# Kernel tuning notes

Measured on AMD Instinct MI355X. Metric: run time of the kernel, lower is better.

## Reference

```python
import jax, jax.numpy as jnp
import numpy as np

NEG_SLOPE = 0.2


def gat_layer(x, src, dst, W, a_src, a_dst, bias, heads, ch, n):
    # x: [N, F_in]; W: [F_in, heads*ch]; a_src/a_dst: [heads, ch]; bias: [heads*ch]
    h = (x @ W).reshape(n, heads, ch)                      # [N, H, C]
    e_src = (h * a_src[None]).sum(-1)                      # [N, H]
    e_dst = (h * a_dst[None]).sum(-1)                      # [N, H]
    e = jax.nn.leaky_relu(e_src[src] + e_dst[dst], NEG_SLOPE)  # [E, H]
    # segment softmax over incoming edges of each dst node
    m = jax.ops.segment_max(e, dst, num_segments=n)        # [N, H]
    e = jnp.exp(e - m[dst])
    denom = jax.ops.segment_sum(e, dst, num_segments=n)    # [N, H]
    alpha = e / (denom[dst] + 1e-16)                       # [E, H]
    msg = h[src] * alpha[:, :, None]                       # [E, H, C]
    out = jax.ops.segment_sum(msg, dst, num_segments=n)    # [N, H, C]
    return out.reshape(n, heads * ch) + bias


def setup_inputs() -> dict:
    key = jax.random.key(0)
    ks = jax.random.split(key, 12)
    N, E, F_IN, C, H = 50000, 1600000, 128, 64, 4
    x = jax.random.normal(ks[0], (N, F_IN), dtype=jnp.float32)
    edge_index = jax.random.randint(ks[1], (2, E), 0, N, dtype=jnp.int32)
    s = 0.1
    return {
        "x": x,
        "edge_index": edge_index,
        "W1": jax.random.normal(ks[2], (F_IN, H * C), dtype=jnp.float32) * s,
        "a_src1": jax.random.normal(ks[3], (H, C), dtype=jnp.float32) * s,
        "a_dst1": jax.random.normal(ks[4], (H, C), dtype=jnp.float32) * s,
        "b1": jnp.zeros((H * C,), dtype=jnp.float32),
        "W2": jax.random.normal(ks[5], (H * C, C), dtype=jnp.float32) * s,
        "a_src2": jax.random.normal(ks[6], (1, C), dtype=jnp.float32) * s,
        "a_dst2": jax.random.normal(ks[7], (1, C), dtype=jnp.float32) * s,
        "b2": jnp.zeros((C,), dtype=jnp.float32),
        "Wout": jax.random.normal(ks[8], (C, 1), dtype=jnp.float32) * s,
        "bout": jnp.zeros((1,), dtype=jnp.float32),
    }


def reference(x, edge_index, W1, a_src1, a_dst1, b1, W2, a_src2, a_dst2, b2, Wout, bout):
    n = x.shape[0]
    # PyG GATConv default add_self_loops=True
    loop = jnp.arange(n, dtype=edge_index.dtype)
    src = jnp.concatenate([edge_index[0], loop])
    dst = jnp.concatenate([edge_index[1], loop])
    h = gat_layer(x, src, dst, W1, a_src1, a_dst1, b1, heads=4, ch=64, n=n)
    h = jax.nn.relu(h)
    h = gat_layer(h, src, dst, W2, a_src2, a_dst2, b2, heads=1, ch=64, n=n)
    h = jax.nn.relu(h)
    logits = (h @ Wout + bout).squeeze(-1)  # [N]
    return logits
```

## Files before the change

### kernel.cpp

```cpp
#include <hip/hip_runtime.h>
#include <hip/hip_bf16.h>

#define NEG_SLOPE 0.2f

using bf16x8 = __attribute__((ext_vector_type(8))) short;
using f32x4  = __attribute__((ext_vector_type(4))) float;

__device__ __forceinline__ unsigned short f2b(float f) {
  unsigned int u = __float_as_uint(f);
  unsigned int r = (u + 0x7FFFu + ((u >> 16) & 1u)) >> 16;
  return (unsigned short)r;
}
__device__ __forceinline__ float b2f(unsigned short v) {
  return __uint_as_float(((unsigned int)v) << 16);
}
__device__ __forceinline__ float leaky_exp(float e) {
  e = e > 0.f ? e : NEG_SLOPE * e;
  return __expf(e);
}

__global__ void k_prep(const float* __restrict__ W1,
                       const float* __restrict__ W2,
                       const float* __restrict__ a_src1,
                       const float* __restrict__ a_dst1,
                       unsigned short* __restrict__ W1h,
                       unsigned short* __restrict__ W1l,
                       unsigned short* __restrict__ W2h,
                       unsigned short* __restrict__ W2l,
                       float* __restrict__ va) {
  int b = blockIdx.x;
  int t = threadIdx.x;
  if (b < 16) {
    int g = b * 256 + t;
    int l = g & 63, tt = (g >> 6) & 3, kc = (g >> 8) & 3, h = (g >> 10) & 3;
    int n = h * 64 + tt * 16 + (l & 15);
    int kbase = kc * 32 + (l >> 4) * 8;
    size_t base = ((((size_t)h * 4 + kc) * 4 + tt) * 64 + l) * 8;
#pragma unroll
    for (int j = 0; j < 8; j++) {
      float v = W1[(size_t)(kbase + j) * 256 + n];
      unsigned short hi = f2b(v);
      W1h[base + j] = hi;
      W1l[base + j] = f2b(v - b2f(hi));
    }
  } else if (b < 24) {
    int g = (b - 16) * 256 + t;
    int l = g & 63, tt = (g >> 6) & 3, kc = (g >> 8) & 7;
    int n = tt * 16 + (l & 15);
    int kbase = kc * 32 + (l >> 4) * 8;
    size_t base = (((size_t)kc * 4 + tt) * 64 + l) * 8;
#pragma unroll
    for (int j = 0; j < 8; j++) {
      float v = W2[(size_t)(kbase + j) * 64 + n];
      unsigned short hi = f2b(v);
      W2h[base + j] = hi;
      W2l[base + j] = f2b(v - b2f(hi));
    }
  } else {
    int g = (b - 24) * 256 + t;
    int k = g >> 3, j = g & 7;
    int h = j & 3;
    const float* a = (j < 4) ? a_src1 : a_dst1;
    float s = 0.f;
    for (int c = 0; c < 64; c++) s += W1[(size_t)k * 256 + h * 64 + c] * a[h * 64 + c];
    va[k * 8 + j] = s;
  }
}

__global__ __launch_bounds__(256) void k_gh_mfma(const unsigned short* __restrict__ Ab,
                                                 const unsigned short* __restrict__ W1h,
                                                 const unsigned short* __restrict__ W1l,
                                                 const float* __restrict__ b1,
                                                 unsigned short* __restrict__ hact_hi,
                                                 unsigned short* __restrict__ hact_lo,
                                                 int M) {
  const int w = threadIdx.x >> 6, l = threadIdx.x & 63;
  const int h = blockIdx.z;
  const int rowA = blockIdx.x * 64 + w * 16 + (l & 15);
  const int rA = rowA < M ? rowA : M - 1;
  const int kg = l >> 4;
  const unsigned short* Aptr = Ab + (size_t)rA * 512 + h * 128 + kg * 8;
  f32x4 acc[4] = {{0.f, 0.f, 0.f, 0.f}, {0.f, 0.f, 0.f, 0.f},
                  {0.f, 0.f, 0.f, 0.f}, {0.f, 0.f, 0.f, 0.f}};
#pragma unroll
  for (int kc = 0; kc < 4; kc++) {
    bf16x8 a = *reinterpret_cast<const bf16x8*>(Aptr + kc * 32);
#pragma unroll
    for (int t = 0; t < 4; t++) {
      size_t base = ((((size_t)h * 4 + kc) * 4 + t) * 64 + l) * 8;
      bf16x8 bh = *reinterpret_cast<const bf16x8*>(W1h + base);
      bf16x8 bl = *reinterpret_cast<const bf16x8*>(W1l + base);
      acc[t] = __builtin_amdgcn_mfma_f32_16x16x32_bf16(a, bh, acc[t], 0, 0, 0);
      acc[t] = __builtin_amdgcn_mfma_f32_16x16x32_bf16(a, bl, acc[t], 0, 0, 0);
    }
  }
  const int orow0 = blockIdx.x * 64 + w * 16 + (l >> 4) * 4;
  const int col16 = l & 15;
#pragma unroll
  for (int t = 0; t < 4; t++) {
    int col = h * 64 + t * 16 + col16;
    float bb = b1[col];
#pragma unroll
    for (int r = 0; r < 4; r++) {
      int row = orow0 + r;
      if (row < M) {
        float v = fmaxf(acc[t][r] + bb, 0.f);
        unsigned short hi = f2b(v);
        hact_hi[(size_t)row * 256 + col] = hi;
        hact_lo[(size_t)row * 256 + col] = f2b(v - b2f(hi));
      }
    }
  }
}

__global__ __launch_bounds__(256) void k_g2_mfma(const unsigned short* __restrict__ Ahi,
                                                 const unsigned short* __restrict__ Alo,
                                                 const unsigned short* __restrict__ W2h,
                                                 const unsigned short* __restrict__ W2l,
                                                 unsigned short* __restrict__ h2b,
                                                 int M) {
  const int w = threadIdx.x >> 6, l = threadIdx.x & 63;
  const int rowA = blockIdx.x * 64 + w * 16 + (l & 15);
  const int rA = rowA < M ? rowA : M - 1;
  const int kg = l >> 4;
  const unsigned short* Ah = Ahi + (size_t)rA * 256 + kg * 8;
  const unsigned short* Al = Alo + (size_t)rA * 256 + kg * 8;
  f32x4 acc[4] = {{0.f, 0.f, 0.f, 0.f}, {0.f, 0.f, 0.f, 0.f},
                  {0.f, 0.f, 0.f, 0.f}, {0.f, 0.f, 0.f, 0.f}};
#pragma unroll
  for (int kc = 0; kc < 8; kc++) {
    bf16x8 ah = *reinterpret_cast<const bf16x8*>(Ah + kc * 32);
    bf16x8 al = *reinterpret_cast<const bf16x8*>(Al + kc * 32);
#pragma unroll
    for (int t = 0; t < 4; t++) {
      size_t base = (((size_t)kc * 4 + t) * 64 + l) * 8;
      bf16x8 bh = *reinterpret_cast<const bf16x8*>(W2h + base);
      bf16x8 bl = *reinterpret_cast<const bf16x8*>(W2l + base);
      acc[t] = __builtin_amdgcn_mfma_f32_16x16x32_bf16(ah, bh, acc[t], 0, 0, 0);
      acc[t] = __builtin_amdgcn_mfma_f32_16x16x32_bf16(ah, bl, acc[t], 0, 0, 0);
      acc[t] = __builtin_amdgcn_mfma_f32_16x16x32_bf16(al, bh, acc[t], 0, 0, 0);
    }
  }
  const int orow0 = blockIdx.x * 64 + w * 16 + (l >> 4) * 4;
  const int col16 = l & 15;
#pragma unroll
  for (int t = 0; t < 4; t++) {
    int col = t * 16 + col16;
#pragma unroll
    for (int r = 0; r < 4; r++) {
      int row = orow0 + r;
      if (row < M) h2b[(size_t)row * 64 + col] = f2b(acc[t][r]);
    }
  }
}

__global__ __launch_bounds__(256) void k_scores_x(const float* __restrict__ x,
                                                  const float* __restrict__ va,
                                                  float* __restrict__ s_src,
                                                  float* __restrict__ s_dst,
                                                  unsigned short* __restrict__ xb,
                                                  int N) {
  int n = blockIdx.x * 4 + (threadIdx.x >> 6);
  if (n >= N) return;
  int lane = threadIdx.x & 63;
  float x0 = x[(size_t)n * 128 + lane];
  float x1 = x[(size_t)n * 128 + 64 + lane];
  xb[(size_t)n * 128 + lane] = f2b(x0);
  xb[(size_t)n * 128 + 64 + lane] = f2b(x1);
  float4 vs0 = *reinterpret_cast<const float4*>(va + lane * 8);
  float4 vd0 = *reinterpret_cast<const float4*>(va + lane * 8 + 4);
  float4 vs1 = *reinterpret_cast<const float4*>(va + (lane + 64) * 8);
  float4 vd1 = *reinterpret_cast<const float4*>(va + (lane + 64) * 8 + 4);
  float rs0 = x0 * vs0.x + x1 * vs1.x, rs1 = x0 * vs0.y + x1 * vs1.y;
  float rs2 = x0 * vs0.z + x1 * vs1.z, rs3 = x0 * vs0.w + x1 * vs1.w;
  float rd0 = x0 * vd0.x + x1 * vd1.x, rd1 = x0 * vd0.y + x1 * vd1.y;
  float rd2 = x0 * vd0.z + x1 * vd1.z, rd3 = x0 * vd0.w + x1 * vd1.w;
#pragma unroll
  for (int off = 32; off; off >>= 1) {
    rs0 += __shfl_xor(rs0, off, 64); rs1 += __shfl_xor(rs1, off, 64);
    rs2 += __shfl_xor(rs2, off, 64); rs3 += __shfl_xor(rs3, off, 64);
    rd0 += __shfl_xor(rd0, off, 64); rd1 += __shfl_xor(rd1, off, 64);
    rd2 += __shfl_xor(rd2, off, 64); rd3 += __shfl_xor(rd3, off, 64);
  }
  if (lane == 0) {
    float4 ss = {rs0, rs1, rs2, rs3};
    float4 dd = {rd0, rd1, rd2, rd3};
    *reinterpret_cast<float4*>(s_src + (size_t)n * 4) = ss;
    *reinterpret_cast<float4*>(s_dst + (size_t)n * 4) = dd;
  }
}

__global__ __launch_bounds__(256) void k_scores2(const unsigned short* __restrict__ h2b,
                                                 const float* __restrict__ a_src,
                                                 const float* __restrict__ a_dst,
                                                 float* __restrict__ s_src,
                                                 float* __restrict__ s_dst,
                                                 int N) {
  int n = blockIdx.x * 4 + (threadIdx.x >> 6);
  if (n >= N) return;
  int lane = threadIdx.x & 63;
  float hv = b2f(h2b[(size_t)n * 64 + lane]);
  float sv = hv * a_src[lane];
  float dv = hv * a_dst[lane];
#pragma unroll
  for (int off = 32; off; off >>= 1) {
    sv += __shfl_xor(sv, off, 64);
    dv += __shfl_xor(dv, off, 64);
  }
  if (lane == 0) {
    s_src[n] = sv;
    s_dst[n] = dv;
  }
}

__global__ void k_histA(const int* __restrict__ ei, int E, int Etot,
                        int* __restrict__ ghist) {
  __shared__ int lh[256];
  int t = threadIdx.x;
  lh[t] = 0;
  __syncthreads();
  int base = (blockIdx.x * 256 + t) * 8;
#pragma unroll
  for (int j = 0; j < 8; j++) {
    int e = base + j;
    if (e < Etot) {
      int dst = (e < E) ? ei[E + e] : (e - E);
      atomicAdd(&lh[dst >> 8], 1);
    }
  }
  __syncthreads();
  if (lh[t]) atomicAdd(&ghist[t], lh[t]);
}

__global__ __launch_bounds__(256) void k_scan196(const int* __restrict__ ghist,
                                                 int* __restrict__ bstart,
                                                 int* __restrict__ gcur,
                                                 int nbuck, int Etot) {
  __shared__ int ws[4];
  int t = threadIdx.x;
  int lane = t & 63, wid = t >> 6;
  int v = (t < nbuck) ? ghist[t] : 0;
  int x = v;
#pragma unroll
  for (int off = 1; off < 64; off <<= 1) {
    int y = __shfl_up(x, off, 64);
    if (lane >= off) x += y;
  }
  if (lane == 63) ws[wid] = x;
  __syncthreads();
  if (t == 0) {
    int a0 = ws[0], a1 = ws[1], a2 = ws[2];
    ws[0] = 0; ws[1] = a0; ws[2] = a0 + a1; ws[3] = a0 + a1 + a2;
  }
  __syncthreads();
  int excl = x - v + ws[wid];
  if (t < nbuck) {
    bstart[t] = excl;
    gcur[t] = excl;
  }
  if (t == 0) bstart[nbuck] = Etot;
}

__global__ void k_scatterA(const int* __restrict__ ei, int E, int Etot,
                           int* __restrict__ gcur,
                           int* __restrict__ keys1,
                           int* __restrict__ vals1) {
  __shared__ int lh[256];
  int t = threadIdx.x;
  lh[t] = 0;
  __syncthreads();
  int base = (blockIdx.x * 256 + t) * 8;
  int dsts[8], srcs[8];
#pragma unroll
  for (int j = 0; j < 8; j++) {
    int e = base + j;
    if (e < Etot) {
      int d, s;
      if (e < E) { d = ei[E + e]; s = ei[e]; }
      else       { d = s = e - E; }
      dsts[j] = d; srcs[j] = s;
      atomicAdd(&lh[d >> 8], 1);
    } else dsts[j] = -1;
  }
  __syncthreads();
  {
    int c = lh[t];
    lh[t] = c ? atomicAdd(&gcur[t], c) : 0;
  }
  __syncthreads();
#pragma unroll
  for (int j = 0; j < 8; j++) {
    if (dsts[j] >= 0) {
      int pos = atomicAdd(&lh[dsts[j] >> 8], 1);
      keys1[pos] = dsts[j];
      vals1[pos] = srcs[j];
    }
  }
}

__global__ __launch_bounds__(256) void k_sortB(const int* __restrict__ keys1,
                                               const int* __restrict__ vals1,
                                               const int* __restrict__ bstart,
                                               int* __restrict__ src_sorted,
                                               int* __restrict__ row_ptr,
                                               int N, int Etot) {
  __shared__ int lh[256];
  __shared__ int ws[4];
  int b = blockIdx.x;
  int t = threadIdx.x;
  int lane = t & 63, wid = t >> 6;
  int s = bstart[b], e2 = bstart[b + 1];
  lh[t] = 0;
  __syncthreads();
  for (int p = s + t; p < e2; p += 256)
    atomicAdd(&lh[keys1[p] & 255], 1);
  __syncthreads();
  int v = lh[t];
  int x = v;
#pragma unroll
  for (int off = 1; off < 64; off <<= 1) {
    int y = __shfl_up(x, off, 64);
    if (lane >= off) x += y;
  }
  if (lane == 63) ws[wid] = x;
  __syncthreads();
  if (t == 0) {
    int a0 = ws[0], a1 = ws[1], a2 = ws[2];
    ws[0] = 0; ws[1] = a0; ws[2] = a0 + a1; ws[3] = a0 + a1 + a2;
  }
  __syncthreads();
  int excl = x - v + ws[wid];
  int dst = (b << 8) + t;
  if (dst < N) row_ptr[dst] = s + excl;
  __syncthreads();
  lh[t] = s + excl;
  __syncthreads();
  for (int p = s + t; p < e2; p += 256) {
    int k = keys1[p] & 255;
    int pos = atomicAdd(&lh[k], 1);
    src_sorted[pos] = vals1[p];
  }
  if (b == 0 && t == 0) row_ptr[N] = Etot;
}

__global__ __launch_bounds__(256) void k_w1csr(const int* __restrict__ row_ptr,
                                               const int* __restrict__ src_sorted,
                                               const float* __restrict__ s_src,
                                               const float* __restrict__ s_dst,
                                               float4* __restrict__ w1s, int N) {
  int n = blockIdx.x * 4 + (threadIdx.x >> 6);
  if (n >= N) return;
  int lane = threadIdx.x & 63;
  float4 sd = *reinterpret_cast<const float4*>(s_dst + (size_t)n * 4);
  int beg = row_ptr[n], end = row_ptr[n + 1];
  for (int p = beg + lane; p < end; p += 64) {
    int s = src_sorted[p];
    float4 ss = *reinterpret_cast<const float4*>(s_src + (size_t)s * 4);
    float4 w;
    w.x = leaky_exp(ss.x + sd.x);
    w.y = leaky_exp(ss.y + sd.y);
    w.z = leaky_exp(ss.z + sd.z);
    w.w = leaky_exp(ss.w + sd.w);
    w1s[p] = w;
  }
}

__global__ __launch_bounds__(256) void k_w2csr(const int* __restrict__ row_ptr,
                                               const int* __restrict__ src_sorted,
                                               const float* __restrict__ s2s,
                                               const float* __restrict__ s2d,
                                               float* __restrict__ w2s, int N) {
  int n = blockIdx.x * 4 + (threadIdx.x >> 6);
  if (n >= N) return;
  int lane = threadIdx.x & 63;
  float sdn = s2d[n];
  int beg = row_ptr[n], end = row_ptr[n + 1];
  for (int p = beg + lane; p < end; p += 64) {
    w2s[p] = leaky_exp(s2s[src_sorted[p]] + sdn);
  }
}

__global__ __launch_bounds__(256) void k_aggx(const unsigned short* __restrict__ xb,
                                              const int* __restrict__ row_ptr,
                                              const int* __restrict__ src_sorted,
                                              const float4* __restrict__ w1s,
                                              unsigned short* __restrict__ avgxb,
                                              int N) {
  int n = blockIdx.x * 4 + (threadIdx.x >> 6);
  if (n >= N) return;
  int lane = threadIdx.x & 63;
  int beg = row_ptr[n], end = row_ptr[n + 1];
  float acc[4][2] = {};
  float wsum[4] = {};
  int p = beg;
  for (; p + 4 <= end; p += 4) {
    int s[4];
    float4 w[4];
    unsigned int pk[4];
#pragma unroll
    for (int j = 0; j < 4; j++) s[j] = src_sorted[p + j];
#pragma unroll
    for (int j = 0; j < 4; j++) w[j] = w1s[p + j];
#pragma unroll
    for (int j = 0; j < 4; j++)
      pk[j] = *reinterpret_cast<const unsigned int*>(xb + (size_t)s[j] * 128 + lane * 2);
#pragma unroll
    for (int j = 0; j < 4; j++) {
      float x0 = __uint_as_float(pk[j] << 16);
      float x1 = __uint_as_float(pk[j] & 0xFFFF0000u);
      acc[0][0] = fmaf(w[j].x, x0, acc[0][0]); acc[0][1] = fmaf(w[j].x, x1, acc[0][1]);
      acc[1][0] = fmaf(w[j].y, x0, acc[1][0]); acc[1][1] = fmaf(w[j].y, x1, acc[1][1]);
      acc[2][0] = fmaf(w[j].z, x0, acc[2][0]); acc[2][1] = fmaf(w[j].z, x1, acc[2][1]);
      acc[3][0] = fmaf(w[j].w, x0, acc[3][0]); acc[3][1] = fmaf(w[j].w, x1, acc[3][1]);
      wsum[0] += w[j].x; wsum[1] += w[j].y; wsum[2] += w[j].z; wsum[3] += w[j].w;
    }
  }
  for (; p < end; p++) {
    int s = src_sorted[p];
    float4 w = w1s[p];
    unsigned int pk = *reinterpret_cast<const unsigned int*>(xb + (size_t)s * 128 + lane * 2);
    float x0 = __uint_as_float(pk << 16);
    float x1 = __uint_as_float(pk & 0xFFFF0000u);
    acc[0][0] = fmaf(w.x, x0, acc[0][0]); acc[0][1] = fmaf(w.x, x1, acc[0][1]);
    acc[1][0] = fmaf(w.y, x0, acc[1][0]); acc[1][1] = fmaf(w.y, x1, acc[1][1]);
    acc[2][0] = fmaf(w.z, x0, acc[2][0]); acc[2][1] = fmaf(w.z, x1, acc[2][1]);
    acc[3][0] = fmaf(w.w, x0, acc[3][0]); acc[3][1] = fmaf(w.w, x1, acc[3][1]);
    wsum[0] += w.x; wsum[1] += w.y; wsum[2] += w.z; wsum[3] += w.w;
  }
#pragma unroll
  for (int h = 0; h < 4; h++) {
    float inv = 1.f / (wsum[h] + 1e-16f);
    unsigned int pk = ((unsigned int)f2b(acc[h][1] * inv) << 16) | f2b(acc[h][0] * inv);
    *reinterpret_cast<unsigned int*>(avgxb + (size_t)n * 512 + h * 128 + lane * 2) = pk;
  }
}

__global__ __launch_bounds__(256) void k_agg2(const unsigned short* __restrict__ h2b,
                                              const int* __restrict__ row_ptr,
                                              const int* __restrict__ src_sorted,
                                              const float* __restrict__ w2s,
                                              const float* __restrict__ bias,
                                              const float* __restrict__ Wout,
                                              const float* __restrict__ bout,
                                              float* __restrict__ logits, int N) {
  int n = blockIdx.x * 4 + (threadIdx.x >> 6);
  if (n >= N) return;
  int lane = threadIdx.x & 63;
  int beg = row_ptr[n], end = row_ptr[n + 1];
  float acc = 0.f, wsum = 0.f;
  int p = beg;
  for (; p + 8 <= end; p += 8) {
    int s[8];
    float w[8];
    unsigned short hv[8];
#pragma unroll
    for (int j = 0; j < 8; j++) s[j] = src_sorted[p + j];
#pragma unroll
    for (int j = 0; j < 8; j++) w[j] = w2s[p + j];
#pragma unroll
    for (int j = 0; j < 8; j++) hv[j] = h2b[(size_t)s[j] * 64 + lane];
#pragma unroll
    for (int j = 0; j < 8; j++) {
      acc = fmaf(w[j], b2f(hv[j]), acc);
      wsum += w[j];
    }
  }
  for (; p < end; p++) {
    float w = w2s[p];
    acc = fmaf(w, b2f(h2b[(size_t)src_sorted[p] * 64 + lane]), acc);
    wsum += w;
  }
  float o = fmaxf(acc / (wsum + 1e-16f) + bias[lane], 0.f);
  float v = o * Wout[lane];
#pragma unroll
  for (int off = 32; off; off >>= 1) v += __shfl_xor(v, off, 64);
  if (lane == 0) logits[n] = v + bout[0];
}

extern "C" void kernel_launch(void* const* d_in, const int* in_sizes, int n_in,
                              void* d_out, int out_size, void* d_ws, size_t ws_size,
                              hipStream_t stream) {
  const float* x      = (const float*)d_in[0];
  const int*   ei     = (const int*)d_in[1];
  const float* W1     = (const float*)d_in[2];
  const float* a_src1 = (const float*)d_in[3];
  const float* a_dst1 = (const float*)d_in[4];
  const float* b1     = (const float*)d_in[5];
  const float* W2     = (const float*)d_in[6];
  const float* a_src2 = (const float*)d_in[7];
  const float* a_dst2 = (const float*)d_in[8];
  const float* b2     = (const float*)d_in[9];
  const float* Wout   = (const float*)d_in[10];
  const float* bout   = (const float*)d_in[11];
  float* logits = (float*)d_out;

  const int HC1  = in_sizes[5];
  const int F_IN = in_sizes[2] / HC1;
  const int N    = in_sizes[0] / F_IN;
  const int E    = in_sizes[1] / 2;
  const int Etot = E + N;
  const int NBUCK = (N + 255) >> 8;

  char* w = (char*)d_ws;
  auto alloc = [&](size_t bytes) {
    char* p = w;
    w += (bytes + 255) & ~(size_t)255;
    return p;
  };
  char* regA = alloc((size_t)N * 128 * sizeof(unsigned short));
  unsigned short* xb = (unsigned short*)regA;
  char* regB = alloc((size_t)N * 512 * sizeof(unsigned short));
  unsigned short* avgxb = (unsigned short*)regB;
  unsigned short* h2b = (unsigned short*)regB;
  float* w2s = (float*)(regB + (size_t)N * 256 * sizeof(unsigned short));
  char* regC = alloc((size_t)N * 256 * 4);
  int* keys1 = (int*)regC;
  int* vals1 = (int*)(regC + (size_t)Etot * 4 + 256);
  float4* w1s = (float4*)regC;
  unsigned short* hact_hi = (unsigned short*)regC;
  unsigned short* hact_lo = (unsigned short*)(regC + (size_t)N * 256 * sizeof(unsigned short));
  float* s_src1  = (float*)alloc((size_t)N * 4 * 4);
  float* s_dst1  = (float*)alloc((size_t)N * 4 * 4);
  float* s2_src  = (float*)alloc((size_t)N * 4);
  float* s2_dst  = (float*)alloc((size_t)N * 4);
  float* va      = (float*)alloc(128 * 8 * 4);
  unsigned short* W1h = (unsigned short*)alloc(4096 * 8 * 2);
  unsigned short* W1l = (unsigned short*)alloc(4096 * 8 * 2);
  unsigned short* W2h = (unsigned short*)alloc(2048 * 8 * 2);
  unsigned short* W2l = (unsigned short*)alloc(2048 * 8 * 2);
  int* row_ptr   = (int*)alloc((size_t)(N + 1) * 4);
  int* src_sorted= (int*)alloc((size_t)Etot * 4);
  int* ghist     = (int*)alloc(256 * 4);
  int* bstart    = (int*)alloc(260 * 4);
  int* gcur      = (int*)alloc(256 * 4);

  hipMemsetAsync(ghist, 0, 256 * 4, stream);

  k_prep<<<28, 256, 0, stream>>>(W1, W2, a_src1, a_dst1, W1h, W1l, W2h, W2l, va);
  k_scores_x<<<(N + 3) / 4, 256, 0, stream>>>(x, va, s_src1, s_dst1, xb, N);

  const int gsort = (Etot + 2047) / 2048;
  k_histA<<<gsort, 256, 0, stream>>>(ei, E, Etot, ghist);
  k_scan196<<<1, 256, 0, stream>>>(ghist, bstart, gcur, NBUCK, Etot);
  k_scatterA<<<gsort, 256, 0, stream>>>(ei, E, Etot, gcur, keys1, vals1);
  k_sortB<<<NBUCK, 256, 0, stream>>>(keys1, vals1, bstart, src_sorted, row_ptr, N, Etot);

  k_w1csr<<<(N + 3) / 4, 256, 0, stream>>>(row_ptr, src_sorted, s_src1, s_dst1, w1s, N);
  k_aggx<<<(N + 3) / 4, 256, 0, stream>>>(xb, row_ptr, src_sorted, w1s, avgxb, N);
  dim3 gh((N + 63) / 64, 1, 4);
  k_gh_mfma<<<gh, 256, 0, stream>>>(avgxb, W1h, W1l, b1, hact_hi, hact_lo, N);

  k_g2_mfma<<<(N + 63) / 64, 256, 0, stream>>>(hact_hi, hact_lo, W2h, W2l, h2b, N);
  k_scores2<<<(N + 3) / 4, 256, 0, stream>>>(h2b, a_src2, a_dst2, s2_src, s2_dst, N);
  k_w2csr<<<(N + 3) / 4, 256, 0, stream>>>(row_ptr, src_sorted, s2_src, s2_dst, w2s, N);
  k_agg2<<<(N + 3) / 4, 256, 0, stream>>>(h2b, row_ptr, src_sorted, w2s,
                                          b2, Wout, bout, logits, N);
}
```

Before: 425.3 us.

## Fuse histogram into scores kernel, pre-normalize attention weights, widen aggx unroll

Drops the memset by zeroing the histogram inside k_prep, and merges the destination histogram into the x-scores kernel as extra blocks, removing two launches. The edge-weight kernels now compute the per-node softmax denominator with a wave reduction and write normalized weights. This takes the weight sums and divides out of both aggregation loops, at the cost of a second pass over the weights (cached in registers for up to 256 edges). The layer-1 aggregation unroll goes from 4 to 8 edges to expose more memory-level parallelism.

```diff
diff --git a/kernel.cpp b/kernel.cpp
--- a/kernel.cpp
+++ b/kernel.cpp
@@ -27,7 +27,8 @@
                        unsigned short* __restrict__ W1l,
                        unsigned short* __restrict__ W2h,
                        unsigned short* __restrict__ W2l,
-                       float* __restrict__ va) {
+                       float* __restrict__ va,
+                       int* __restrict__ ghist) {
   int b = blockIdx.x;
   int t = threadIdx.x;
   if (b < 16) {
@@ -56,7 +57,7 @@
       W2h[base + j] = hi;
       W2l[base + j] = f2b(v - b2f(hi));
     }
-  } else {
+  } else if (b < 28) {
     int g = (b - 24) * 256 + t;
     int k = g >> 3, j = g & 7;
     int h = j & 3;
@@ -64,6 +65,8 @@
     float s = 0.f;
     for (int c = 0; c < 64; c++) s += W1[(size_t)k * 256 + h * 64 + c] * a[h * 64 + c];
     va[k * 8 + j] = s;
+  } else {
+    ghist[t] = 0;
   }
 }
 
@@ -154,12 +157,33 @@
   }
 }
 
-__global__ __launch_bounds__(256) void k_scores_x(const float* __restrict__ x,
-                                                  const float* __restrict__ va,
-                                                  float* __restrict__ s_src,
-                                                  float* __restrict__ s_dst,
-                                                  unsigned short* __restrict__ xb,
-                                                  int N) {
+__global__ __launch_bounds__(256) void k_sxh(const float* __restrict__ x,
+                                             const float* __restrict__ va,
+                                             float* __restrict__ s_src,
+                                             float* __restrict__ s_dst,
+                                             unsigned short* __restrict__ xb,
+                                             int N, int nsx,
+                                             const int* __restrict__ ei,
+                                             int E, int Etot,
+                                             int* __restrict__ ghist) {
+  __shared__ int lh[256];
+  if (blockIdx.x >= nsx) {
+    int t = threadIdx.x;
+    lh[t] = 0;
+    __syncthreads();
+    int base = ((blockIdx.x - nsx) * 256 + t) * 8;
+#pragma unroll
+    for (int j = 0; j < 8; j++) {
+      int e = base + j;
+      if (e < Etot) {
+        int dst = (e < E) ? ei[E + e] : (e - E);
+        atomicAdd(&lh[dst >> 8], 1);
+      }
+    }
+    __syncthreads();
+    if (lh[t]) atomicAdd(&ghist[t], lh[t]);
+    return;
+  }
   int n = blockIdx.x * 4 + (threadIdx.x >> 6);
   if (n >= N) return;
   int lane = threadIdx.x & 63;
@@ -213,25 +237,6 @@
   }
 }
 
-__global__ void k_histA(const int* __restrict__ ei, int E, int Etot,
-                        int* __restrict__ ghist) {
-  __shared__ int lh[256];
-  int t = threadIdx.x;
-  lh[t] = 0;
-  __syncthreads();
-  int base = (blockIdx.x * 256 + t) * 8;
-#pragma unroll
-  for (int j = 0; j < 8; j++) {
-    int e = base + j;
-    if (e < Etot) {
-      int dst = (e < E) ? ei[E + e] : (e - E);
-      atomicAdd(&lh[dst >> 8], 1);
-    }
-  }
-  __syncthreads();
-  if (lh[t]) atomicAdd(&ghist[t], lh[t]);
-}
-
 __global__ __launch_bounds__(256) void k_scan196(const int* __restrict__ ghist,
                                                  int* __restrict__ bstart,
                                                  int* __restrict__ gcur,
@@ -343,17 +348,20 @@
   if (b == 0 && t == 0) row_ptr[N] = Etot;
 }
 
-__global__ __launch_bounds__(256) void k_w1csr(const int* __restrict__ row_ptr,
-                                               const int* __restrict__ src_sorted,
-                                               const float* __restrict__ s_src,
-                                               const float* __restrict__ s_dst,
-                                               float4* __restrict__ w1s, int N) {
+__global__ __launch_bounds__(256) void k_w1n(const int* __restrict__ row_ptr,
+                                             const int* __restrict__ src_sorted,
+                                             const float* __restrict__ s_src,
+                                             const float* __restrict__ s_dst,
+                                             float4* __restrict__ w1s, int N) {
   int n = blockIdx.x * 4 + (threadIdx.x >> 6);
   if (n >= N) return;
   int lane = threadIdx.x & 63;
   float4 sd = *reinterpret_cast<const float4*>(s_dst + (size_t)n * 4);
   int beg = row_ptr[n], end = row_ptr[n + 1];
-  for (int p = beg + lane; p < end; p += 64) {
+  float4 wreg[4];
+  float sx = 0.f, sy = 0.f, sz = 0.f, sw = 0.f;
+  int i = 0;
+  for (int p = beg + lane; p < end; p += 64, i++) {
     int s = src_sorted[p];
     float4 ss = *reinterpret_cast<const float4*>(s_src + (size_t)s * 4);
     float4 w;
@@ -361,22 +369,49 @@
     w.y = leaky_exp(ss.y + sd.y);
     w.z = leaky_exp(ss.z + sd.z);
     w.w = leaky_exp(ss.w + sd.w);
+    if (i < 4) wreg[i] = w; else w1s[p] = w;
+    sx += w.x; sy += w.y; sz += w.z; sw += w.w;
+  }
+#pragma unroll
+  for (int off = 32; off; off >>= 1) {
+    sx += __shfl_xor(sx, off, 64); sy += __shfl_xor(sy, off, 64);
+    sz += __shfl_xor(sz, off, 64); sw += __shfl_xor(sw, off, 64);
+  }
+  float ix = 1.f / (sx + 1e-16f), iy = 1.f / (sy + 1e-16f);
+  float iz = 1.f / (sz + 1e-16f), iw = 1.f / (sw + 1e-16f);
+  i = 0;
+  for (int p = beg + lane; p < end; p += 64, i++) {
+    float4 w = (i < 4) ? wreg[i] : w1s[p];
+    w.x *= ix; w.y *= iy; w.z *= iz; w.w *= iw;
     w1s[p] = w;
   }
 }
 
-__global__ __launch_bounds__(256) void k_w2csr(const int* __restrict__ row_ptr,
-                                               const int* __restrict__ src_sorted,
-                                               const float* __restrict__ s2s,
-                                               const float* __restrict__ s2d,
-                                               float* __restrict__ w2s, int N) {
+__global__ __launch_bounds__(256) void k_w2n(const int* __restrict__ row_ptr,
+                                             const int* __restrict__ src_sorted,
+                                             const float* __restrict__ s2s,
+                                             const float* __restrict__ s2d,
+                                             float* __restrict__ w2s, int N) {
   int n = blockIdx.x * 4 + (threadIdx.x >> 6);
   if (n >= N) return;
   int lane = threadIdx.x & 63;
   float sdn = s2d[n];
   int beg = row_ptr[n], end = row_ptr[n + 1];
-  for (int p = beg + lane; p < end; p += 64) {
-    w2s[p] = leaky_exp(s2s[src_sorted[p]] + sdn);
+  float wreg[4];
+  float sum = 0.f;
+  int i = 0;
+  for (int p = beg + lane; p < end; p += 64, i++) {
+    float w = leaky_exp(s2s[src_sorted[p]] + sdn);
+    if (i < 4) wreg[i] = w; else w2s[p] = w;
+    sum += w;
+  }
+#pragma unroll
+  for (int off = 32; off; off >>= 1) sum += __shfl_xor(sum, off, 64);
+  float inv = 1.f / (sum + 1e-16f);
+  i = 0;
+  for (int p = beg + lane; p < end; p += 64, i++) {
+    float w = (i < 4) ? wreg[i] : w2s[p];
+    w2s[p] = w * inv;
   }
 }
 
@@ -391,28 +426,26 @@
   int lane = threadIdx.x & 63;
   int beg = row_ptr[n], end = row_ptr[n + 1];
   float acc[4][2] = {};
-  float wsum[4] = {};
   int p = beg;
-  for (; p + 4 <= end; p += 4) {
-    int s[4];
-    float4 w[4];
-    unsigned int pk[4];
-#pragma unroll
-    for (int j = 0; j < 4; j++) s[j] = src_sorted[p + j];
-#pragma unroll
-    for (int j = 0; j < 4; j++) w[j] = w1s[p + j];
-#pragma unroll
-    for (int j = 0; j < 4; j++)
+  for (; p + 8 <= end; p += 8) {
+    int s[8];
+    float4 w[8];
+    unsigned int pk[8];
+#pragma unroll
+    for (int j = 0; j < 8; j++) s[j] = src_sorted[p + j];
+#pragma unroll
+    for (int j = 0; j < 8; j++) w[j] = w1s[p + j];
+#pragma unroll
+    for (int j = 0; j < 8; j++)
       pk[j] = *reinterpret_cast<const unsigned int*>(xb + (size_t)s[j] * 128 + lane * 2);
 #pragma unroll
-    for (int j = 0; j < 4; j++) {
+    for (int j = 0; j < 8; j++) {
       float x0 = __uint_as_float(pk[j] << 16);
       float x1 = __uint_as_float(pk[j] & 0xFFFF0000u);
       acc[0][0] = fmaf(w[j].x, x0, acc[0][0]); acc[0][1] = fmaf(w[j].x, x1, acc[0][1]);
       acc[1][0] = fmaf(w[j].y, x0, acc[1][0]); acc[1][1] = fmaf(w[j].y, x1, acc[1][1]);
       acc[2][0] = fmaf(w[j].z, x0, acc[2][0]); acc[2][1] = fmaf(w[j].z, x1, acc[2][1]);
       acc[3][0] = fmaf(w[j].w, x0, acc[3][0]); acc[3][1] = fmaf(w[j].w, x1, acc[3][1]);
-      wsum[0] += w[j].x; wsum[1] += w[j].y; wsum[2] += w[j].z; wsum[3] += w[j].w;
     }
   }
   for (; p < end; p++) {
@@ -425,12 +458,10 @@
     acc[1][0] = fmaf(w.y, x0, acc[1][0]); acc[1][1] = fmaf(w.y, x1, acc[1][1]);
     acc[2][0] = fmaf(w.z, x0, acc[2][0]); acc[2][1] = fmaf(w.z, x1, acc[2][1]);
     acc[3][0] = fmaf(w.w, x0, acc[3][0]); acc[3][1] = fmaf(w.w, x1, acc[3][1]);
-    wsum[0] += w.x; wsum[1] += w.y; wsum[2] += w.z; wsum[3] += w.w;
   }
 #pragma unroll
   for (int h = 0; h < 4; h++) {
-    float inv = 1.f / (wsum[h] + 1e-16f);
-    unsigned int pk = ((unsigned int)f2b(acc[h][1] * inv) << 16) | f2b(acc[h][0] * inv);
+    unsigned int pk = ((unsigned int)f2b(acc[h][1]) << 16) | f2b(acc[h][0]);
     *reinterpret_cast<unsigned int*>(avgxb + (size_t)n * 512 + h * 128 + lane * 2) = pk;
   }
 }
@@ -447,7 +478,7 @@
   if (n >= N) return;
   int lane = threadIdx.x & 63;
   int beg = row_ptr[n], end = row_ptr[n + 1];
-  float acc = 0.f, wsum = 0.f;
+  float acc = 0.f;
   int p = beg;
   for (; p + 8 <= end; p += 8) {
     int s[8];
@@ -460,17 +491,11 @@
 #pragma unroll
     for (int j = 0; j < 8; j++) hv[j] = h2b[(size_t)s[j] * 64 + lane];
 #pragma unroll
-    for (int j = 0; j < 8; j++) {
-      acc = fmaf(w[j], b2f(hv[j]), acc);
-      wsum += w[j];
-    }
-  }
-  for (; p < end; p++) {
-    float w = w2s[p];
-    acc = fmaf(w, b2f(h2b[(size_t)src_sorted[p] * 64 + lane]), acc);
-    wsum += w;
-  }
-  float o = fmaxf(acc / (wsum + 1e-16f) + bias[lane], 0.f);
+    for (int j = 0; j < 8; j++) acc = fmaf(w[j], b2f(hv[j]), acc);
+  }
+  for (; p < end; p++)
+    acc = fmaf(w2s[p], b2f(h2b[(size_t)src_sorted[p] * 64 + lane]), acc);
+  float o = fmaxf(acc + bias[lane], 0.f);
   float v = o * Wout[lane];
 #pragma unroll
   for (int off = 32; off; off >>= 1) v += __shfl_xor(v, off, 64);
@@ -534,25 +559,26 @@
   int* bstart    = (int*)alloc(260 * 4);
   int* gcur      = (int*)alloc(256 * 4);
 
-  hipMemsetAsync(ghist, 0, 256 * 4, stream);
-
-  k_prep<<<28, 256, 0, stream>>>(W1, W2, a_src1, a_dst1, W1h, W1l, W2h, W2l, va);
-  k_scores_x<<<(N + 3) / 4, 256, 0, stream>>>(x, va, s_src1, s_dst1, xb, N);
-
+  k_prep<<<29, 256, 0, stream>>>(W1, W2, a_src1, a_dst1, W1h, W1l, W2h, W2l,
+                                 va, ghist);
+
+  const int nsx = (N + 3) / 4;
   const int gsort = (Etot + 2047) / 2048;
-  k_histA<<<gsort, 256, 0, stream>>>(ei, E, Etot, ghist);
+  k_sxh<<<nsx + gsort, 256, 0, stream>>>(x, va, s_src1, s_dst1, xb, N, nsx,
+                                         ei, E, Etot, ghist);
+
   k_scan196<<<1, 256, 0, stream>>>(ghist, bstart, gcur, NBUCK, Etot);
   k_scatterA<<<gsort, 256, 0, stream>>>(ei, E, Etot, gcur, keys1, vals1);
   k_sortB<<<NBUCK, 256, 0, stream>>>(keys1, vals1, bstart, src_sorted, row_ptr, N, Etot);
 
-  k_w1csr<<<(N + 3) / 4, 256, 0, stream>>>(row_ptr, src_sorted, s_src1, s_dst1, w1s, N);
+  k_w1n<<<(N + 3) / 4, 256, 0, stream>>>(row_ptr, src_sorted, s_src1, s_dst1, w1s, N);
   k_aggx<<<(N + 3) / 4, 256, 0, stream>>>(xb, row_ptr, src_sorted, w1s, avgxb, N);
   dim3 gh((N + 63) / 64, 1, 4);
   k_gh_mfma<<<gh, 256, 0, stream>>>(avgxb, W1h, W1l, b1, hact_hi, hact_lo, N);
 
   k_g2_mfma<<<(N + 63) / 64, 256, 0, stream>>>(hact_hi, hact_lo, W2h, W2l, h2b, N);
   k_scores2<<<(N + 3) / 4, 256, 0, stream>>>(h2b, a_src2, a_dst2, s2_src, s2_dst, N);
-  k_w2csr<<<(N + 3) / 4, 256, 0, stream>>>(row_ptr, src_sorted, s2_src, s2_dst, w2s, N);
+  k_w2n<<<(N + 3) / 4, 256, 0, stream>>>(row_ptr, src_sorted, s2_src, s2_dst, w2s, N);
   k_agg2<<<(N + 3) / 4, 256, 0, stream>>>(h2b, row_ptr, src_sorted, w2s,
                                           b2, Wout, bout, logits, N);
 }
```

After: 420.0 us. Within noise of the previous version (-1.2%).
